# Kernel tuning notes

Hardware: AMD Instinct MI355X
Metric: run time of the kernel (lower is better)

Reference implementation:

```python
import jax, jax.numpy as jnp
import numpy as np

MAX_FLOW = 80.0
STEPS = 200
STEP_SIZE = 10.0
EPS = 1e-5
NOISE_STD = 0.05
GRAD_CLIP = 0.03


def _energy(flow, img1, img2, log_weights):
    # flow: (B,2,H,W), img1/img2: (B,3,H,W); returns per-sample energy (B,)
    _, _, H, W = img1.shape
    flow = flow * MAX_FLOW
    img1 = (img1 + 1.0) / 2.0
    img2 = (img2 + 1.0) / 2.0
    A = jnp.sum((img1 - img2) ** 2, axis=1)                       # (B,H,W)
    data_term = jnp.sum(jnp.sqrt(A + EPS), axis=(1, 2))           # (B,)
    # kernel_dx/_dy are per-channel [-1,1] finite differences -> slicing
    dx = flow[:, :, :, 1:] - flow[:, :, :, :-1]                   # (B,2,H,W-1)
    dy = flow[:, :, 1:, :] - flow[:, :, :-1, :]                   # (B,2,H-1,W)
    Bx = jnp.pad(jnp.sum(dx ** 2, axis=1), ((0, 0), (0, 0), (0, 1)))
    By = jnp.pad(jnp.sum(dy ** 2, axis=1), ((0, 0), (0, 1), (0, 0)))
    smooth_term = jnp.sum(jnp.sqrt(Bx + By + EPS), axis=(1, 2))   # (B,)
    out = jnp.exp(log_weights[0]) * data_term + jnp.exp(log_weights[1]) * smooth_term
    return out / (H * W)


def _langevin_sample(init, img2, log_weights, key):
    # 200-step Langevin MCMC: noise inject, clamp, energy grad, clipped update, clamp
    def energy_sum(x):
        flow, img1 = x[:, :2], x[:, 2:]
        return jnp.sum(_energy(flow, img1, img2, log_weights))

    grad_fn = jax.grad(energy_sum)

    def step(x, k):
        noise = NOISE_STD * jax.random.normal(k, x.shape, x.dtype)
        x = jnp.clip(x + noise, -1.0, 1.0)
        g = jnp.clip(grad_fn(x), -GRAD_CLIP, GRAD_CLIP)
        x = jnp.clip(x - STEP_SIZE * g, -1.0, 1.0)
        return x, None

    keys = jax.random.split(key, STEPS)
    x, _ = jax.lax.scan(step, init, keys)
    return x


def setup_inputs() -> dict:
    key = jax.random.key(0)
    k1, k2, k3, k4 = jax.random.split(key, 4)
    B, H, W = 8, 384, 512
    target1 = jax.random.normal(k1, (B, 2, H, W), dtype=jnp.float32)
    input1 = jax.random.uniform(k2, (B, 3, H, W), dtype=jnp.float32)
    input2 = jax.random.uniform(k3, (B, 3, H, W), dtype=jnp.float32)
    init = jax.random.uniform(k4, (B, 5, H, W), dtype=jnp.float32) * 2.0 - 1.0
    log_weights = jnp.ones((2,), dtype=jnp.float32)
    return {"target1": target1, "input1": input1, "input2": input2,
            "init": init, "log_weights": log_weights}


def reference(target1, input1, input2, init, log_weights):
    flow_pos = target1 / MAX_FLOW
    img1_pos = input1 * 2.0 - 1.0
    img2 = input2 * 2.0 - 1.0
    # negative samples via Langevin MCMC; detached as in the torch module
    neg = jax.lax.stop_gradient(_langevin_sample(init, img2, log_weights, jax.random.key(1)))
    flow_neg, img1_neg = neg[:, :2], neg[:, 2:]
    pos_energy = _energy(flow_pos, img1_pos, img2, log_weights)
    neg_energy = _energy(flow_neg, img1_neg, img2, log_weights)
    energies = jnp.stack([pos_energy, neg_energy])  # (2,B)
    return energies, flow_neg * MAX_FLOW, (img1_neg + 1.0) / 2.0
```

## Files before the change

### kernel.cpp

```cpp
#include <hip/hip_runtime.h>
#include <math.h>

#define HH 384
#define WW 512
#define HW 196608
#define QHW 49152
#define CHW 983040
#define NTOT 7864320
#define FLOW_N 3145728
#define OUT_FLOW_OFF 16
#define OUT_IMG_OFF (16 + FLOW_N)
#define EPS_F 1e-5f
#define EPS_S (1e-5f / 6400.0f)
#define INV_HW (1.0f/196608.0f)

__device__ __forceinline__ float rsq_f(float x)  { return __builtin_amdgcn_rsqf(x); }
__device__ __forceinline__ float ln_f(float x)   { return 0.69314718055994531f * __builtin_amdgcn_logf(x); }
__device__ __forceinline__ float sqrt_f(float x) { return __builtin_amdgcn_sqrtf(x); }
__device__ __forceinline__ float med3(float x, float lo, float hi) {
  return __builtin_amdgcn_fmed3f(x, lo, hi);
}

__host__ __device__ __forceinline__ void tf2x32(unsigned k0, unsigned k1,
                                                unsigned x0, unsigned x1,
                                                unsigned& o0, unsigned& o1) {
  const unsigned ks2 = k0 ^ k1 ^ 0x1BD11BDAu;
  x0 += k0; x1 += k1;
#define TFR(r) x0 += x1; x1 = (x1 << (r)) | (x1 >> (32 - (r))); x1 ^= x0;
  TFR(13) TFR(15) TFR(26) TFR(6)
  x0 += k1;  x1 += ks2 + 1u;
  TFR(17) TFR(29) TFR(16) TFR(24)
  x0 += ks2; x1 += k0 + 2u;
  TFR(13) TFR(15) TFR(26) TFR(6)
  x0 += k0;  x1 += k1 + 3u;
  TFR(17) TFR(29) TFR(16) TFR(24)
  x0 += k1;  x1 += ks2 + 4u;
  TFR(13) TFR(15) TFR(26) TFR(6)
  x0 += ks2; x1 += k0 + 5u;
#undef TFR
  o0 = x0; o1 = x1;
}

__device__ __forceinline__ float noise_from_bits(unsigned bits) {
  const float LO = -0.99999994f;
  float f = __uint_as_float((bits >> 9) | 0x3F800000u) - 1.0f;
  float u = fmaxf(LO, f * 2.0f + LO);
  float w = -ln_f((1.0f - u) * (1.0f + u));
  float p;
  if (w < 5.0f) {
    w -= 2.5f;
    p = 2.81022636e-08f;
    p = p * w + 3.43273939e-07f;
    p = p * w + -3.5233877e-06f;
    p = p * w + -4.39150654e-06f;
    p = p * w + 0.00021858087f;
    p = p * w + -0.00125372503f;
    p = p * w + -0.00417768164f;
    p = p * w + 0.246640727f;
    p = p * w + 1.50140941f;
  } else {
    w = sqrt_f(w) - 3.0f;
    p = -0.000200214257f;
    p = p * w + 0.000100950558f;
    p = p * w + 0.00134934322f;
    p = p * w + -0.00367342844f;
    p = p * w + 0.00573950773f;
    p = p * w + -0.0076224613f;
    p = p * w + 0.00943887047f;
    p = p * w + 1.00167406f;
    p = p * w + 2.83297682f;
  }
  float z = 1.4142135623730951f * (p * u);
  return 0.05f * z;
}

__device__ __forceinline__ float upd(float x, float g) {
  g = med3(g, -0.03f, 0.03f);
  return med3(x - 10.0f * g, -1.0f, 1.0f);
}

__device__ __forceinline__ float noise_at(unsigned ka, unsigned kb, unsigned idx) {
  unsigned o0, o1;
  tf2x32(ka, kb, 0u, idx, o0, o1);
  return noise_from_bits(o0 ^ o1);
}

__device__ __forceinline__ float clip1(float x) { return med3(x, -1.0f, 1.0f); }

__device__ __forceinline__ void noise_store4(float* dst, const float xn[4],
                                             unsigned ka, unsigned kb, unsigned idx0) {
  float r[4];
#pragma unroll
  for (int j = 0; j < 4; ++j)
    r[j] = clip1(xn[j] + noise_at(ka, kb, idx0 + (unsigned)j));
  *(float4*)dst = make_float4(r[0], r[1], r[2], r[3]);
}

__global__ void k_init(double* acc, float* sw, const float* lw) {
  int t = threadIdx.x;
  if (t < 32) acc[t] = 0.0;
  if (t == 32) {
    sw[0] = expf(lw[0]) * INV_HW * 0.5f;
    sw[1] = expf(lw[1]) * INV_HW * 80.0f;
  }
}

__global__ __launch_bounds__(256) void k_fnoise0(const float* __restrict__ init,
    float* __restrict__ Y, unsigned ka, unsigned kb) {
  int e = blockIdx.x * 256 + threadIdx.x;
  int b = e / (2 * HW);
  int r = e - b * 2 * HW;
  int orig = b * CHW + r;
  Y[e] = clip1(init[orig] + noise_at(ka, kb, (unsigned)orig));
}

template <bool FINAL>
__global__ __launch_bounds__(256) void k_fstep4(const float* __restrict__ X,
    float* __restrict__ Y, const float* __restrict__ sw,
    unsigned ka, unsigned kb) {
  int tid = blockIdx.x * 256 + threadIdx.x;
  int b = tid / QHW;
  int q = tid - b * QHW;
  int p = q * 4;
  int h = p >> 9, w = p & 511;
  float s1v = sw[1];
  const float* F0 = X + b * 2 * HW;
  const float* F1 = F0 + HW;
  const bool wpos = (w > 0), wend = (w == 508);
  const bool hpos = (h > 0), hlast = (h == 383);

  float cf[2][5], fm1[2], dw[2][4], dwm1[2], uf[2][5];
  {
    float4 a0 = *(const float4*)(F0 + p);
    float4 a1 = *(const float4*)(F1 + p);
    cf[0][0]=a0.x; cf[0][1]=a0.y; cf[0][2]=a0.z; cf[0][3]=a0.w;
    cf[1][0]=a1.x; cf[1][1]=a1.y; cf[1][2]=a1.z; cf[1][3]=a1.w;
    cf[0][4] = wend ? cf[0][3] : F0[p + 4];
    cf[1][4] = wend ? cf[1][3] : F1[p + 4];
    fm1[0] = wpos ? F0[p - 1] : cf[0][0];
    fm1[1] = wpos ? F1[p - 1] : cf[1][0];
    if (!hlast) {
      float4 d0 = *(const float4*)(F0 + p + WW);
      float4 d1 = *(const float4*)(F1 + p + WW);
      dw[0][0]=d0.x; dw[0][1]=d0.y; dw[0][2]=d0.z; dw[0][3]=d0.w;
      dw[1][0]=d1.x; dw[1][1]=d1.y; dw[1][2]=d1.z; dw[1][3]=d1.w;
      dwm1[0] = wpos ? F0[p + WW - 1] : fm1[0];
      dwm1[1] = wpos ? F1[p + WW - 1] : fm1[1];
    } else {
#pragma unroll
      for (int c = 0; c < 2; ++c) {
        for (int j = 0; j < 4; ++j) dw[c][j] = cf[c][j];
        dwm1[c] = fm1[c];
      }
    }
    if (hpos) {
      float4 u0 = *(const float4*)(F0 + p - WW);
      float4 u1 = *(const float4*)(F1 + p - WW);
      uf[0][0]=u0.x; uf[0][1]=u0.y; uf[0][2]=u0.z; uf[0][3]=u0.w;
      uf[1][0]=u1.x; uf[1][1]=u1.y; uf[1][2]=u1.z; uf[1][3]=u1.w;
      uf[0][4] = wend ? uf[0][3] : F0[p - WW + 4];
      uf[1][4] = wend ? uf[1][3] : F1[p - WW + 4];
    } else {
#pragma unroll
      for (int c = 0; c < 2; ++c)
        for (int j = 0; j < 5; ++j) uf[c][j] = cf[c][j];
    }
  }

  float dxc[2][4], dyc[2][4], invSc[4], dxu[2][4], dyu[2][4], invSu[4];
  float dxl[2], dyl[2], invSL;
#pragma unroll
  for (int j = 0; j < 4; ++j) {
#pragma unroll
    for (int c = 0; c < 2; ++c) {
      dxc[c][j] = cf[c][j + 1] - cf[c][j];
      dyc[c][j] = dw[c][j] - cf[c][j];
      dxu[c][j] = uf[c][j + 1] - uf[c][j];
      dyu[c][j] = cf[c][j] - uf[c][j];
    }
    invSc[j] = rsq_f(dxc[0][j]*dxc[0][j] + dxc[1][j]*dxc[1][j]
                   + dyc[0][j]*dyc[0][j] + dyc[1][j]*dyc[1][j] + EPS_S);
    invSu[j] = rsq_f(dxu[0][j]*dxu[0][j] + dxu[1][j]*dxu[1][j]
                   + dyu[0][j]*dyu[0][j] + dyu[1][j]*dyu[1][j] + EPS_S);
  }
  dxl[0] = cf[0][0] - fm1[0];  dxl[1] = cf[1][0] - fm1[1];
  dyl[0] = dwm1[0] - fm1[0];   dyl[1] = dwm1[1] - fm1[1];
  invSL = rsq_f(dxl[0]*dxl[0] + dxl[1]*dxl[1]
              + dyl[0]*dyl[0] + dyl[1]*dyl[1] + EPS_S);

  float xnF[2][4];
#pragma unroll
  for (int j = 0; j < 4; ++j) {
#pragma unroll
    for (int c = 0; c < 2; ++c) {
      float g = -(dxc[c][j] + dyc[c][j]) * invSc[j];
      if (j == 0) { if (wpos) g += dxl[c] * invSL; }
      else        { g += dxc[c][j - 1] * invSc[j - 1]; }
      if (hpos)   { g += dyu[c][j] * invSu[j]; }
      xnF[c][j] = upd(cf[c][j], g * s1v);
    }
  }

  if (!FINAL) {
    int nbase = b * CHW + p;
    int sb = b * 2 * HW + p;
    noise_store4(Y + sb,      xnF[0], ka, kb, (unsigned)nbase);
    noise_store4(Y + sb + HW, xnF[1], ka, kb, (unsigned)(nbase + HW));
  } else {
    float* outF = Y + OUT_FLOW_OFF + b * 2 * HW;
    *(float4*)(outF + p)      = make_float4(xnF[0][0]*80.f, xnF[0][1]*80.f,
                                            xnF[0][2]*80.f, xnF[0][3]*80.f);
    *(float4*)(outF + HW + p) = make_float4(xnF[1][0]*80.f, xnF[1][1]*80.f,
                                            xnF[1][2]*80.f, xnF[1][3]*80.f);
  }
}

__global__ __launch_bounds__(256, 8) void k_img(const float* __restrict__ init,
    const float* __restrict__ in2, const float* __restrict__ sw,
    float* __restrict__ out) {
  __shared__ unsigned Kl[404];
  int tid = threadIdx.x;
  if (tid < 202) {
    unsigned a, bb;
    tf2x32(0u, 1u, 0u, (unsigned)tid, a, bb);
    Kl[2 * tid] = a; Kl[2 * tid + 1] = bb;
  }
  __syncthreads();
  int g = blockIdx.x * 256 + tid;
  int b = g / HW;
  int p = g - b * HW;
  float s0 = sw[0];
  unsigned base = (unsigned)(b * CHW + 2 * HW + p);
  float x0 = init[base], x1 = init[base + HW], x2 = init[base + 2 * HW];
  const float* I2 = in2 + b * 3 * HW + p;
  float i0 = ((I2[0] * 2.0f - 1.0f) + 1.0f) * 0.5f;
  float i1 = ((I2[HW] * 2.0f - 1.0f) + 1.0f) * 0.5f;
  float i2v = ((I2[2 * HW] * 2.0f - 1.0f) + 1.0f) * 0.5f;

  unsigned ka = Kl[0], kb = Kl[1];
  for (int t = 0; t < 200; ++t) {
    unsigned kan = Kl[2 * t + 2], kbn = Kl[2 * t + 3];
    x0 = clip1(x0 + noise_at(ka, kb, base));
    x1 = clip1(x1 + noise_at(ka, kb, base + HW));
    x2 = clip1(x2 + noise_at(ka, kb, base + 2 * HW));
    float d0 = (x0 + 1.0f) * 0.5f - i0;
    float d1 = (x1 + 1.0f) * 0.5f - i1;
    float d2 = (x2 + 1.0f) * 0.5f - i2v;
    float A = d0*d0 + d1*d1 + d2*d2;
    float sI = s0 * rsq_f(A + EPS_F);
    x0 = upd(x0, d0 * sI);
    x1 = upd(x1, d1 * sI);
    x2 = upd(x2, d2 * sI);
    ka = kan; kb = kbn;
  }
  float* outI = out + OUT_IMG_OFF + b * 3 * HW + p;
  outI[0]      = (x0 + 1.0f) * 0.5f;
  outI[HW]     = (x1 + 1.0f) * 0.5f;
  outI[2 * HW] = (x2 + 1.0f) * 0.5f;
}

__device__ __forceinline__ void block_acc2(double v0, double v1, double* a0, double* a1) {
  for (int off = 32; off > 0; off >>= 1) {
    v0 += __shfl_down(v0, off, 64);
    v1 += __shfl_down(v1, off, 64);
  }
  __shared__ double s0m[4], s1m[4];
  int lane = threadIdx.x & 63, wv = threadIdx.x >> 6;
  if (lane == 0) { s0m[wv] = v0; s1m[wv] = v1; }
  __syncthreads();
  if (threadIdx.x == 0) {
    atomicAdd(a0, s0m[0] + s0m[1] + s0m[2] + s0m[3]);
    atomicAdd(a1, s1m[0] + s1m[1] + s1m[2] + s1m[3]);
  }
}

__global__ __launch_bounds__(256) void k_pos_energy(const float* __restrict__ t1,
    const float* __restrict__ in1, const float* __restrict__ in2,
    double* __restrict__ acc) {
  int blk = blockIdx.x;
  int b = blk / 96;
  int local = blk - b * 96;
  const float* T0 = t1 + b * 2 * HW;
  const float* T1 = T0 + HW;
  const float* I1 = in1 + b * 3 * HW;
  const float* I2 = in2 + b * 3 * HW;
  double data = 0.0, smooth = 0.0;
  for (int it = 0; it < 8; ++it) {
    int p = (local * 8 + it) * 256 + threadIdx.x;
    int h = p >> 9, w = p & 511;
    float f00 = (T0[p] / 80.0f) * 80.0f;
    float f10 = (T1[p] / 80.0f) * 80.0f;
    float dx0 = 0, dx1 = 0, dy0 = 0, dy1 = 0;
    if (w < 511) { dx0 = (T0[p+1]/80.0f)*80.0f - f00;  dx1 = (T1[p+1]/80.0f)*80.0f - f10; }
    if (h < 383) { dy0 = (T0[p+WW]/80.0f)*80.0f - f00; dy1 = (T1[p+WW]/80.0f)*80.0f - f10; }
    smooth += (double)sqrtf(dx0*dx0 + dx1*dx1 + dy0*dy0 + dy1*dy1 + EPS_F);
    float d0 = ((I1[p]*2.0f-1.0f)+1.0f)*0.5f        - ((I2[p]*2.0f-1.0f)+1.0f)*0.5f;
    float d1 = ((I1[p+HW]*2.0f-1.0f)+1.0f)*0.5f     - ((I2[p+HW]*2.0f-1.0f)+1.0f)*0.5f;
    float d2 = ((I1[p+2*HW]*2.0f-1.0f)+1.0f)*0.5f   - ((I2[p+2*HW]*2.0f-1.0f)+1.0f)*0.5f;
    data += (double)sqrtf(d0*d0 + d1*d1 + d2*d2 + EPS_F);
  }
  block_acc2(data, smooth, &acc[b], &acc[8 + b]);
}

__global__ __launch_bounds__(256) void k_neg_energy(const float* __restrict__ out,
    const float* __restrict__ in2, double* __restrict__ acc) {
  int blk = blockIdx.x;
  int b = blk / 96;
  int local = blk - b * 96;
  const float* F0 = out + OUT_FLOW_OFF + b * 2 * HW;
  const float* F1 = F0 + HW;
  const float* I = out + OUT_IMG_OFF + b * 3 * HW;
  const float* I2 = in2 + b * 3 * HW;
  double data = 0.0, smooth = 0.0;
  for (int it = 0; it < 8; ++it) {
    int p = (local * 8 + it) * 256 + threadIdx.x;
    int h = p >> 9, w = p & 511;
    float f00 = F0[p], f10 = F1[p];
    float dx0 = 0, dx1 = 0, dy0 = 0, dy1 = 0;
    if (w < 511) { dx0 = F0[p + 1] - f00;  dx1 = F1[p + 1] - f10; }
    if (h < 383) { dy0 = F0[p + WW] - f00; dy1 = F1[p + WW] - f10; }
    smooth += (double)sqrtf(dx0*dx0 + dx1*dx1 + dy0*dy0 + dy1*dy1 + EPS_F);
    float d0 = I[p]        - ((I2[p]*2.0f-1.0f)+1.0f)*0.5f;
    float d1 = I[p+HW]     - ((I2[p+HW]*2.0f-1.0f)+1.0f)*0.5f;
    float d2 = I[p+2*HW]   - ((I2[p+2*HW]*2.0f-1.0f)+1.0f)*0.5f;
    data += (double)sqrtf(d0*d0 + d1*d1 + d2*d2 + EPS_F);
  }
  block_acc2(data, smooth, &acc[16 + b], &acc[24 + b]);
}

__global__ void k_finalize(const double* __restrict__ acc,
                           const float* __restrict__ lw, float* __restrict__ out) {
  int t = threadIdx.x;
  if (t < 16) {
    int b = t & 7, neg = t >> 3;
    double data   = acc[neg * 16 + b];
    double smooth = acc[neg * 16 + 8 + b];
    double e0 = exp((double)lw[0]), e1 = exp((double)lw[1]);
    out[t] = (float)((e0 * data + e1 * smooth) / 196608.0);
  }
}

extern "C" void kernel_launch(void* const* d_in, const int* in_sizes, int n_in,
                              void* d_out, int out_size, void* d_ws, size_t ws_size,
                              hipStream_t stream) {
  const float* t1  = (const float*)d_in[0];
  const float* in1 = (const float*)d_in[1];
  const float* in2 = (const float*)d_in[2];
  const float* init = (const float*)d_in[3];
  const float* lw  = (const float*)d_in[4];
  float* out = (float*)d_out;

  double* acc = (double*)d_ws;
  float* sw = (float*)((char*)d_ws + 256);
  float* bufFA = (float*)((char*)d_ws + 2048);
  size_t need = 2048 + 2 * (size_t)FLOW_N * sizeof(float);
  float* bufFB = (ws_size >= need) ? bufFA + FLOW_N
                                   : out + OUT_FLOW_OFF;

  unsigned K0[200], K1[200];
  for (int t = 0; t < 200; ++t) tf2x32(0u, 1u, 0u, (unsigned)t, K0[t], K1[t]);

  k_init<<<1, 64, 0, stream>>>(acc, sw, lw);
  k_pos_energy<<<8 * 96, 256, 0, stream>>>(t1, in1, in2, acc);

  k_fnoise0<<<FLOW_N / 256, 256, 0, stream>>>(init, bufFB, K0[0], K1[0]);
  for (int t = 0; t < 199; ++t) {
    const float* src = (t % 2 == 0) ? bufFB : bufFA;
    float* dst       = (t % 2 == 0) ? bufFA : bufFB;
    k_fstep4<false><<<8 * QHW / 256, 256, 0, stream>>>(src, dst, sw,
                                                       K0[t + 1], K1[t + 1]);
  }
  k_fstep4<true><<<8 * QHW / 256, 256, 0, stream>>>(bufFA, out, sw, 0u, 0u);

  k_img<<<8 * HW / 256, 256, 0, stream>>>(init, in2, sw, out);

  k_neg_energy<<<8 * 96, 256, 0, stream>>>(out, in2, acc);
  k_finalize<<<1, 64, 0, stream>>>(acc, lw, out);
}
```

Before: 5.127 ms.

## Process three pixels per thread in image Langevin kernel and remap flow-step blocks

The image-channel Langevin kernel now handles three pixels per thread with one third as many threads, and moves the per-step Threefry keys into scalar registers via readfirstlane, so the key work is amortised and the independent chains give more instruction-level parallelism. The flow-step kernel permutes block indices so consecutive blocks land in different batch or image regions, presumably to spread them across XCDs and their L2 caches. The risk is higher register pressure and fewer waves for the image kernel, and the block permutation may not help cache locality.

```diff
diff --git a/kernel.cpp b/kernel.cpp
--- a/kernel.cpp
+++ b/kernel.cpp
@@ -8,6 +8,8 @@
 #define CHW 983040
 #define NTOT 7864320
 #define FLOW_N 3145728
+#define NQUADS 393216
+#define IMG_NT 524288
 #define OUT_FLOW_OFF 16
 #define OUT_IMG_OFF (16 + FLOW_N)
 #define EPS_F 1e-5f
@@ -118,7 +120,8 @@
 __global__ __launch_bounds__(256) void k_fstep4(const float* __restrict__ X,
     float* __restrict__ Y, const float* __restrict__ sw,
     unsigned ka, unsigned kb) {
-  int tid = blockIdx.x * 256 + threadIdx.x;
+  int wb = (blockIdx.x & 7) * (NQUADS / 256 / 8) + (blockIdx.x >> 3);
+  int tid = wb * 256 + threadIdx.x;
   int b = tid / QHW;
   int q = tid - b * QHW;
   int p = q * 4;
@@ -227,36 +230,56 @@
   }
   __syncthreads();
   int g = blockIdx.x * 256 + tid;
-  int b = g / HW;
-  int p = g - b * HW;
   float s0 = sw[0];
-  unsigned base = (unsigned)(b * CHW + 2 * HW + p);
-  float x0 = init[base], x1 = init[base + HW], x2 = init[base + 2 * HW];
-  const float* I2 = in2 + b * 3 * HW + p;
-  float i0 = ((I2[0] * 2.0f - 1.0f) + 1.0f) * 0.5f;
-  float i1 = ((I2[HW] * 2.0f - 1.0f) + 1.0f) * 0.5f;
-  float i2v = ((I2[2 * HW] * 2.0f - 1.0f) + 1.0f) * 0.5f;
-
-  unsigned ka = Kl[0], kb = Kl[1];
+
+  int px[3] = { g, g + IMG_NT, g + 2 * IMG_NT };
+  unsigned base[3];
+  float x[3][3], it2[3][3];
+#pragma unroll
+  for (int k = 0; k < 3; ++k) {
+    int b = px[k] / HW;
+    int p = px[k] - b * HW;
+    base[k] = (unsigned)(b * CHW + 2 * HW + p);
+    const float* I2 = in2 + b * 3 * HW + p;
+#pragma unroll
+    for (int c = 0; c < 3; ++c) {
+      x[k][c] = init[base[k] + c * HW];
+      it2[k][c] = ((I2[c * HW] * 2.0f - 1.0f) + 1.0f) * 0.5f;
+    }
+  }
+
+  unsigned ka = __builtin_amdgcn_readfirstlane(Kl[0]);
+  unsigned kb = __builtin_amdgcn_readfirstlane(Kl[1]);
   for (int t = 0; t < 200; ++t) {
     unsigned kan = Kl[2 * t + 2], kbn = Kl[2 * t + 3];
-    x0 = clip1(x0 + noise_at(ka, kb, base));
-    x1 = clip1(x1 + noise_at(ka, kb, base + HW));
-    x2 = clip1(x2 + noise_at(ka, kb, base + 2 * HW));
-    float d0 = (x0 + 1.0f) * 0.5f - i0;
-    float d1 = (x1 + 1.0f) * 0.5f - i1;
-    float d2 = (x2 + 1.0f) * 0.5f - i2v;
-    float A = d0*d0 + d1*d1 + d2*d2;
-    float sI = s0 * rsq_f(A + EPS_F);
-    x0 = upd(x0, d0 * sI);
-    x1 = upd(x1, d1 * sI);
-    x2 = upd(x2, d2 * sI);
-    ka = kan; kb = kbn;
-  }
-  float* outI = out + OUT_IMG_OFF + b * 3 * HW + p;
-  outI[0]      = (x0 + 1.0f) * 0.5f;
-  outI[HW]     = (x1 + 1.0f) * 0.5f;
-  outI[2 * HW] = (x2 + 1.0f) * 0.5f;
+#pragma unroll
+    for (int k = 0; k < 3; ++k) {
+      float n0 = noise_at(ka, kb, base[k]);
+      float n1 = noise_at(ka, kb, base[k] + (unsigned)HW);
+      float n2 = noise_at(ka, kb, base[k] + 2u * (unsigned)HW);
+      float y0 = clip1(x[k][0] + n0);
+      float y1 = clip1(x[k][1] + n1);
+      float y2 = clip1(x[k][2] + n2);
+      float d0 = (y0 + 1.0f) * 0.5f - it2[k][0];
+      float d1 = (y1 + 1.0f) * 0.5f - it2[k][1];
+      float d2 = (y2 + 1.0f) * 0.5f - it2[k][2];
+      float sI = s0 * rsq_f(d0 * d0 + d1 * d1 + d2 * d2 + EPS_F);
+      x[k][0] = upd(y0, d0 * sI);
+      x[k][1] = upd(y1, d1 * sI);
+      x[k][2] = upd(y2, d2 * sI);
+    }
+    ka = __builtin_amdgcn_readfirstlane(kan);
+    kb = __builtin_amdgcn_readfirstlane(kbn);
+  }
+#pragma unroll
+  for (int k = 0; k < 3; ++k) {
+    int b = px[k] / HW;
+    int p = px[k] - b * HW;
+    float* outI = out + OUT_IMG_OFF + b * 3 * HW + p;
+#pragma unroll
+    for (int c = 0; c < 3; ++c)
+      outI[c * HW] = (x[k][c] + 1.0f) * 0.5f;
+  }
 }
 
 __device__ __forceinline__ void block_acc2(double v0, double v1, double* a0, double* a1) {
@@ -367,12 +390,12 @@
   for (int t = 0; t < 199; ++t) {
     const float* src = (t % 2 == 0) ? bufFB : bufFA;
     float* dst       = (t % 2 == 0) ? bufFA : bufFB;
-    k_fstep4<false><<<8 * QHW / 256, 256, 0, stream>>>(src, dst, sw,
-                                                       K0[t + 1], K1[t + 1]);
-  }
-  k_fstep4<true><<<8 * QHW / 256, 256, 0, stream>>>(bufFA, out, sw, 0u, 0u);
-
-  k_img<<<8 * HW / 256, 256, 0, stream>>>(init, in2, sw, out);
+    k_fstep4<false><<<NQUADS / 256, 256, 0, stream>>>(src, dst, sw,
+                                                      K0[t + 1], K1[t + 1]);
+  }
+  k_fstep4<true><<<NQUADS / 256, 256, 0, stream>>>(bufFA, out, sw, 0u, 0u);
+
+  k_img<<<IMG_NT / 256, 256, 0, stream>>>(init, in2, sw, out);
 
   k_neg_energy<<<8 * 96, 256, 0, stream>>>(out, in2, acc);
   k_finalize<<<1, 64, 0, stream>>>(acc, lw, out);
```

After: 4.666 ms. 1.1x faster.

## Fuse image-channel Langevin steps into per-step flow kernel launches

Applied to the files above, without the earlier changes.

The separate 200-iteration register-resident image kernel is removed. Each of the 200 per-step launches now runs extra blocks that advance the three image channels by one step, reading and writing state through the output buffer. Flow blocks are also remapped with an interleaved block index. The aim is to hide the long serial image kernel inside the flow launches, which are bandwidth-bound and short. The cost is that the image state now makes a global memory round trip on every step instead of staying in registers.

```diff
diff --git a/kernel.cpp b/kernel.cpp
--- a/kernel.cpp
+++ b/kernel.cpp
@@ -6,8 +6,10 @@
 #define HW 196608
 #define QHW 49152
 #define CHW 983040
-#define NTOT 7864320
 #define FLOW_N 3145728
+#define NQUADS 393216
+#define NBF 1536
+#define NBI 1536
 #define OUT_FLOW_OFF 16
 #define OUT_IMG_OFF (16 + FLOW_N)
 #define EPS_F 1e-5f
@@ -87,7 +89,7 @@
 
 __device__ __forceinline__ float clip1(float x) { return med3(x, -1.0f, 1.0f); }
 
-__device__ __forceinline__ void noise_store4(float* dst, const float xn[4],
+__device__ __forceinline__ void noise_store4(float* dst, const float* xn,
                                              unsigned ka, unsigned kb, unsigned idx0) {
   float r[4];
 #pragma unroll
@@ -115,148 +117,157 @@
 }
 
 template <bool FINAL>
-__global__ __launch_bounds__(256) void k_fstep4(const float* __restrict__ X,
-    float* __restrict__ Y, const float* __restrict__ sw,
-    unsigned ka, unsigned kb) {
-  int tid = blockIdx.x * 256 + threadIdx.x;
-  int b = tid / QHW;
-  int q = tid - b * QHW;
-  int p = q * 4;
-  int h = p >> 9, w = p & 511;
-  float s1v = sw[1];
-  const float* F0 = X + b * 2 * HW;
-  const float* F1 = F0 + HW;
-  const bool wpos = (w > 0), wend = (w == 508);
-  const bool hpos = (h > 0), hlast = (h == 383);
-
-  float cf[2][5], fm1[2], dw[2][4], dwm1[2], uf[2][5];
-  {
-    float4 a0 = *(const float4*)(F0 + p);
-    float4 a1 = *(const float4*)(F1 + p);
-    cf[0][0]=a0.x; cf[0][1]=a0.y; cf[0][2]=a0.z; cf[0][3]=a0.w;
-    cf[1][0]=a1.x; cf[1][1]=a1.y; cf[1][2]=a1.z; cf[1][3]=a1.w;
-    cf[0][4] = wend ? cf[0][3] : F0[p + 4];
-    cf[1][4] = wend ? cf[1][3] : F1[p + 4];
-    fm1[0] = wpos ? F0[p - 1] : cf[0][0];
-    fm1[1] = wpos ? F1[p - 1] : cf[1][0];
-    if (!hlast) {
-      float4 d0 = *(const float4*)(F0 + p + WW);
-      float4 d1 = *(const float4*)(F1 + p + WW);
-      dw[0][0]=d0.x; dw[0][1]=d0.y; dw[0][2]=d0.z; dw[0][3]=d0.w;
-      dw[1][0]=d1.x; dw[1][1]=d1.y; dw[1][2]=d1.z; dw[1][3]=d1.w;
-      dwm1[0] = wpos ? F0[p + WW - 1] : fm1[0];
-      dwm1[1] = wpos ? F1[p + WW - 1] : fm1[1];
+__global__ __launch_bounds__(256) void k_step(const float* __restrict__ X,
+    float* __restrict__ Y, float* __restrict__ S,
+    const float* __restrict__ init, const float* __restrict__ in2,
+    const float* __restrict__ sw,
+    unsigned fka, unsigned fkb,
+    unsigned ika, unsigned ikb,
+    int first) {
+  if (blockIdx.x < NBF) {
+    int wb = (blockIdx.x & 7) * (NBF / 8) + (blockIdx.x >> 3);
+    int tid = wb * 256 + threadIdx.x;
+    int b = tid / QHW;
+    int q = tid - b * QHW;
+    int p = q * 4;
+    int h = p >> 9, w = p & 511;
+    float s1v = sw[1];
+    const float* F0 = X + b * 2 * HW;
+    const float* F1 = F0 + HW;
+    const bool wpos = (w > 0), wend = (w == 508);
+    const bool hpos = (h > 0), hlast = (h == 383);
+
+    float cf[2][5], fm1[2], dw[2][4], dwm1[2], uf[2][5];
+    {
+      float4 a0 = *(const float4*)(F0 + p);
+      float4 a1 = *(const float4*)(F1 + p);
+      cf[0][0]=a0.x; cf[0][1]=a0.y; cf[0][2]=a0.z; cf[0][3]=a0.w;
+      cf[1][0]=a1.x; cf[1][1]=a1.y; cf[1][2]=a1.z; cf[1][3]=a1.w;
+      cf[0][4] = wend ? cf[0][3] : F0[p + 4];
+      cf[1][4] = wend ? cf[1][3] : F1[p + 4];
+      fm1[0] = wpos ? F0[p - 1] : cf[0][0];
+      fm1[1] = wpos ? F1[p - 1] : cf[1][0];
+      if (!hlast) {
+        float4 d0 = *(const float4*)(F0 + p + WW);
+        float4 d1 = *(const float4*)(F1 + p + WW);
+        dw[0][0]=d0.x; dw[0][1]=d0.y; dw[0][2]=d0.z; dw[0][3]=d0.w;
+        dw[1][0]=d1.x; dw[1][1]=d1.y; dw[1][2]=d1.z; dw[1][3]=d1.w;
+        dwm1[0] = wpos ? F0[p + WW - 1] : fm1[0];
+        dwm1[1] = wpos ? F1[p + WW - 1] : fm1[1];
+      } else {
+#pragma unroll
+        for (int c = 0; c < 2; ++c) {
+          for (int j = 0; j < 4; ++j) dw[c][j] = cf[c][j];
+          dwm1[c] = fm1[c];
+        }
+      }
+      if (hpos) {
+        float4 u0 = *(const float4*)(F0 + p - WW);
+        float4 u1 = *(const float4*)(F1 + p - WW);
+        uf[0][0]=u0.x; uf[0][1]=u0.y; uf[0][2]=u0.z; uf[0][3]=u0.w;
+        uf[1][0]=u1.x; uf[1][1]=u1.y; uf[1][2]=u1.z; uf[1][3]=u1.w;
+        uf[0][4] = wend ? uf[0][3] : F0[p - WW + 4];
+        uf[1][4] = wend ? uf[1][3] : F1[p - WW + 4];
+      } else {
+#pragma unroll
+        for (int c = 0; c < 2; ++c)
+          for (int j = 0; j < 5; ++j) uf[c][j] = cf[c][j];
+      }
+    }
+
+    float dxc[2][4], dyc[2][4], invSc[4], dxu[2][4], dyu[2][4], invSu[4];
+    float dxl[2], dyl[2], invSL;
+#pragma unroll
+    for (int j = 0; j < 4; ++j) {
+#pragma unroll
+      for (int c = 0; c < 2; ++c) {
+        dxc[c][j] = cf[c][j + 1] - cf[c][j];
+        dyc[c][j] = dw[c][j] - cf[c][j];
+        dxu[c][j] = uf[c][j + 1] - uf[c][j];
+        dyu[c][j] = cf[c][j] - uf[c][j];
+      }
+      invSc[j] = rsq_f(dxc[0][j]*dxc[0][j] + dxc[1][j]*dxc[1][j]
+                     + dyc[0][j]*dyc[0][j] + dyc[1][j]*dyc[1][j] + EPS_S);
+      invSu[j] = rsq_f(dxu[0][j]*dxu[0][j] + dxu[1][j]*dxu[1][j]
+                     + dyu[0][j]*dyu[0][j] + dyu[1][j]*dyu[1][j] + EPS_S);
+    }
+    dxl[0] = cf[0][0] - fm1[0];  dxl[1] = cf[1][0] - fm1[1];
+    dyl[0] = dwm1[0] - fm1[0];   dyl[1] = dwm1[1] - fm1[1];
+    invSL = rsq_f(dxl[0]*dxl[0] + dxl[1]*dxl[1]
+                + dyl[0]*dyl[0] + dyl[1]*dyl[1] + EPS_S);
+
+    float xnF[2][4];
+#pragma unroll
+    for (int j = 0; j < 4; ++j) {
+#pragma unroll
+      for (int c = 0; c < 2; ++c) {
+        float g = -(dxc[c][j] + dyc[c][j]) * invSc[j];
+        if (j == 0) { if (wpos) g += dxl[c] * invSL; }
+        else        { g += dxc[c][j - 1] * invSc[j - 1]; }
+        if (hpos)   { g += dyu[c][j] * invSu[j]; }
+        xnF[c][j] = upd(cf[c][j], g * s1v);
+      }
+    }
+
+    if (!FINAL) {
+      int nbase = b * CHW + p;
+      int sb = b * 2 * HW + p;
+      noise_store4(Y + sb,      &xnF[0][0], fka, fkb, (unsigned)nbase);
+      noise_store4(Y + sb + HW, &xnF[1][0], fka, fkb, (unsigned)(nbase + HW));
     } else {
-#pragma unroll
-      for (int c = 0; c < 2; ++c) {
-        for (int j = 0; j < 4; ++j) dw[c][j] = cf[c][j];
-        dwm1[c] = fm1[c];
-      }
-    }
-    if (hpos) {
-      float4 u0 = *(const float4*)(F0 + p - WW);
-      float4 u1 = *(const float4*)(F1 + p - WW);
-      uf[0][0]=u0.x; uf[0][1]=u0.y; uf[0][2]=u0.z; uf[0][3]=u0.w;
-      uf[1][0]=u1.x; uf[1][1]=u1.y; uf[1][2]=u1.z; uf[1][3]=u1.w;
-      uf[0][4] = wend ? uf[0][3] : F0[p - WW + 4];
-      uf[1][4] = wend ? uf[1][3] : F1[p - WW + 4];
-    } else {
-#pragma unroll
-      for (int c = 0; c < 2; ++c)
-        for (int j = 0; j < 5; ++j) uf[c][j] = cf[c][j];
-    }
-  }
-
-  float dxc[2][4], dyc[2][4], invSc[4], dxu[2][4], dyu[2][4], invSu[4];
-  float dxl[2], dyl[2], invSL;
-#pragma unroll
-  for (int j = 0; j < 4; ++j) {
-#pragma unroll
-    for (int c = 0; c < 2; ++c) {
-      dxc[c][j] = cf[c][j + 1] - cf[c][j];
-      dyc[c][j] = dw[c][j] - cf[c][j];
-      dxu[c][j] = uf[c][j + 1] - uf[c][j];
-      dyu[c][j] = cf[c][j] - uf[c][j];
-    }
-    invSc[j] = rsq_f(dxc[0][j]*dxc[0][j] + dxc[1][j]*dxc[1][j]
-                   + dyc[0][j]*dyc[0][j] + dyc[1][j]*dyc[1][j] + EPS_S);
-    invSu[j] = rsq_f(dxu[0][j]*dxu[0][j] + dxu[1][j]*dxu[1][j]
-                   + dyu[0][j]*dyu[0][j] + dyu[1][j]*dyu[1][j] + EPS_S);
-  }
-  dxl[0] = cf[0][0] - fm1[0];  dxl[1] = cf[1][0] - fm1[1];
-  dyl[0] = dwm1[0] - fm1[0];   dyl[1] = dwm1[1] - fm1[1];
-  invSL = rsq_f(dxl[0]*dxl[0] + dxl[1]*dxl[1]
-              + dyl[0]*dyl[0] + dyl[1]*dyl[1] + EPS_S);
-
-  float xnF[2][4];
-#pragma unroll
-  for (int j = 0; j < 4; ++j) {
-#pragma unroll
-    for (int c = 0; c < 2; ++c) {
-      float g = -(dxc[c][j] + dyc[c][j]) * invSc[j];
-      if (j == 0) { if (wpos) g += dxl[c] * invSL; }
-      else        { g += dxc[c][j - 1] * invSc[j - 1]; }
-      if (hpos)   { g += dyu[c][j] * invSu[j]; }
-      xnF[c][j] = upd(cf[c][j], g * s1v);
-    }
-  }
-
-  if (!FINAL) {
-    int nbase = b * CHW + p;
-    int sb = b * 2 * HW + p;
-    noise_store4(Y + sb,      xnF[0], ka, kb, (unsigned)nbase);
-    noise_store4(Y + sb + HW, xnF[1], ka, kb, (unsigned)(nbase + HW));
+      float* outF = Y + OUT_FLOW_OFF + b * 2 * HW;
+      *(float4*)(outF + p)      = make_float4(xnF[0][0]*80.f, xnF[0][1]*80.f,
+                                              xnF[0][2]*80.f, xnF[0][3]*80.f);
+      *(float4*)(outF + HW + p) = make_float4(xnF[1][0]*80.f, xnF[1][1]*80.f,
+                                              xnF[1][2]*80.f, xnF[1][3]*80.f);
+    }
   } else {
-    float* outF = Y + OUT_FLOW_OFF + b * 2 * HW;
-    *(float4*)(outF + p)      = make_float4(xnF[0][0]*80.f, xnF[0][1]*80.f,
-                                            xnF[0][2]*80.f, xnF[0][3]*80.f);
-    *(float4*)(outF + HW + p) = make_float4(xnF[1][0]*80.f, xnF[1][1]*80.f,
-                                            xnF[1][2]*80.f, xnF[1][3]*80.f);
-  }
-}
-
-__global__ __launch_bounds__(256, 8) void k_img(const float* __restrict__ init,
-    const float* __restrict__ in2, const float* __restrict__ sw,
-    float* __restrict__ out) {
-  __shared__ unsigned Kl[404];
-  int tid = threadIdx.x;
-  if (tid < 202) {
-    unsigned a, bb;
-    tf2x32(0u, 1u, 0u, (unsigned)tid, a, bb);
-    Kl[2 * tid] = a; Kl[2 * tid + 1] = bb;
-  }
-  __syncthreads();
-  int g = blockIdx.x * 256 + tid;
-  int b = g / HW;
-  int p = g - b * HW;
-  float s0 = sw[0];
-  unsigned base = (unsigned)(b * CHW + 2 * HW + p);
-  float x0 = init[base], x1 = init[base + HW], x2 = init[base + 2 * HW];
-  const float* I2 = in2 + b * 3 * HW + p;
-  float i0 = ((I2[0] * 2.0f - 1.0f) + 1.0f) * 0.5f;
-  float i1 = ((I2[HW] * 2.0f - 1.0f) + 1.0f) * 0.5f;
-  float i2v = ((I2[2 * HW] * 2.0f - 1.0f) + 1.0f) * 0.5f;
-
-  unsigned ka = Kl[0], kb = Kl[1];
-  for (int t = 0; t < 200; ++t) {
-    unsigned kan = Kl[2 * t + 2], kbn = Kl[2 * t + 3];
-    x0 = clip1(x0 + noise_at(ka, kb, base));
-    x1 = clip1(x1 + noise_at(ka, kb, base + HW));
-    x2 = clip1(x2 + noise_at(ka, kb, base + 2 * HW));
-    float d0 = (x0 + 1.0f) * 0.5f - i0;
-    float d1 = (x1 + 1.0f) * 0.5f - i1;
-    float d2 = (x2 + 1.0f) * 0.5f - i2v;
-    float A = d0*d0 + d1*d1 + d2*d2;
-    float sI = s0 * rsq_f(A + EPS_F);
-    x0 = upd(x0, d0 * sI);
-    x1 = upd(x1, d1 * sI);
-    x2 = upd(x2, d2 * sI);
-    ka = kan; kb = kbn;
-  }
-  float* outI = out + OUT_IMG_OFF + b * 3 * HW + p;
-  outI[0]      = (x0 + 1.0f) * 0.5f;
-  outI[HW]     = (x1 + 1.0f) * 0.5f;
-  outI[2 * HW] = (x2 + 1.0f) * 0.5f;
+    int fb = (int)blockIdx.x - NBF;
+    int wb = (fb & 7) * (NBI / 8) + (fb >> 3);
+    int tid = wb * 256 + threadIdx.x;
+    int b = tid / QHW;
+    int q = tid - b * QHW;
+    int p = q * 4;
+    float s0 = sw[0];
+    float* Sp = S + b * 3 * HW + p;
+    const float* I2 = in2 + b * 3 * HW + p;
+    unsigned nb = (unsigned)(b * CHW + 2 * HW + p);
+
+    float x[3][4], iv[3][4];
+#pragma unroll
+    for (int c = 0; c < 3; ++c) {
+      float4 v = first ? *(const float4*)(init + b * CHW + 2 * HW + c * HW + p)
+                       : *(const float4*)(Sp + c * HW);
+      x[c][0]=v.x; x[c][1]=v.y; x[c][2]=v.z; x[c][3]=v.w;
+      float4 wv = *(const float4*)(I2 + c * HW);
+      iv[c][0] = ((wv.x * 2.0f - 1.0f) + 1.0f) * 0.5f;
+      iv[c][1] = ((wv.y * 2.0f - 1.0f) + 1.0f) * 0.5f;
+      iv[c][2] = ((wv.z * 2.0f - 1.0f) + 1.0f) * 0.5f;
+      iv[c][3] = ((wv.w * 2.0f - 1.0f) + 1.0f) * 0.5f;
+    }
+#pragma unroll
+    for (int j = 0; j < 4; ++j) {
+      float y0 = clip1(x[0][j] + noise_at(ika, ikb, nb + (unsigned)j));
+      float y1 = clip1(x[1][j] + noise_at(ika, ikb, nb + (unsigned)(HW + j)));
+      float y2 = clip1(x[2][j] + noise_at(ika, ikb, nb + (unsigned)(2 * HW + j)));
+      float d0 = (y0 + 1.0f) * 0.5f - iv[0][j];
+      float d1 = (y1 + 1.0f) * 0.5f - iv[1][j];
+      float d2 = (y2 + 1.0f) * 0.5f - iv[2][j];
+      float A = d0*d0 + d1*d1 + d2*d2;
+      float sI = s0 * rsq_f(A + EPS_F);
+      x[0][j] = upd(y0, d0 * sI);
+      x[1][j] = upd(y1, d1 * sI);
+      x[2][j] = upd(y2, d2 * sI);
+    }
+#pragma unroll
+    for (int c = 0; c < 3; ++c) {
+      float4 v;
+      if (!FINAL) v = make_float4(x[c][0], x[c][1], x[c][2], x[c][3]);
+      else v = make_float4((x[c][0]+1.0f)*0.5f, (x[c][1]+1.0f)*0.5f,
+                           (x[c][2]+1.0f)*0.5f, (x[c][3]+1.0f)*0.5f);
+      *(float4*)(Sp + c * HW) = v;
+    }
+  }
 }
 
 __device__ __forceinline__ void block_acc2(double v0, double v1, double* a0, double* a1) {
@@ -356,6 +367,7 @@
   size_t need = 2048 + 2 * (size_t)FLOW_N * sizeof(float);
   float* bufFB = (ws_size >= need) ? bufFA + FLOW_N
                                    : out + OUT_FLOW_OFF;
+  float* imgS = out + OUT_IMG_OFF;
 
   unsigned K0[200], K1[200];
   for (int t = 0; t < 200; ++t) tf2x32(0u, 1u, 0u, (unsigned)t, K0[t], K1[t]);
@@ -367,12 +379,12 @@
   for (int t = 0; t < 199; ++t) {
     const float* src = (t % 2 == 0) ? bufFB : bufFA;
     float* dst       = (t % 2 == 0) ? bufFA : bufFB;
-    k_fstep4<false><<<8 * QHW / 256, 256, 0, stream>>>(src, dst, sw,
-                                                       K0[t + 1], K1[t + 1]);
-  }
-  k_fstep4<true><<<8 * QHW / 256, 256, 0, stream>>>(bufFA, out, sw, 0u, 0u);
-
-  k_img<<<8 * HW / 256, 256, 0, stream>>>(init, in2, sw, out);
+    k_step<false><<<NBF + NBI, 256, 0, stream>>>(src, dst, imgS, init, in2, sw,
+                                                 K0[t + 1], K1[t + 1],
+                                                 K0[t], K1[t], t == 0);
+  }
+  k_step<true><<<NBF + NBI, 256, 0, stream>>>(bufFA, out, imgS, init, in2, sw,
+                                              0u, 0u, K0[199], K1[199], 0);
 
   k_neg_energy<<<8 * 96, 256, 0, stream>>>(out, in2, acc);
   k_finalize<<<1, 64, 0, stream>>>(acc, lw, out);
```

After: 5.107 ms. About the same (-0.4%).
